# Kernel tuning notes

Measured on AMD Instinct MI355X. Metric: run time of the kernel, lower is better.

The kernel has to match this reference:

```python
import jax, jax.numpy as jnp
import numpy as np

B = 262144
N = 1_000_000
R = 64
H = 128


def setup_inputs() -> dict:
    key = jax.random.key(0)
    k1, k2, k3, k4, k5, k6 = jax.random.split(key, 6)
    return {
        "x": jax.random.randint(k1, (B,), 0, N),
        "y": jax.random.randint(k2, (B,), 0, N),
        "r": jax.random.randint(k3, (B,), 0, R),
        "l": jax.random.randint(k4, (B,), 0, 2),
        "Wx": jax.random.normal(k5, (N, H), dtype=jnp.float32),
        "Wr": jax.random.normal(k6, (R, H), dtype=jnp.float32),
    }


def reference(x, y, r, l, Wx, Wr):
    # one_hot(idx) @ W  ==  gather rows  (same math, no dense GEMM)
    embx = Wx[x]          # [B, H]
    emby = Wx[y]          # [B, H]
    embr = Wr[r]          # [B, H]

    # regulartion: sigmoid'(clamp(embr))
    s = jax.nn.sigmoid(jnp.clip(embr, -6.0, 6.0))
    re_embr = s * (1.0 - s)

    preds = jax.nn.sigmoid(jnp.sum(embx * emby * re_embr, axis=1))[:, None]  # [B,1]
    logits = jnp.concatenate([preds, 1.0 - preds], axis=1)                   # [B,2]

    # torch.nn.CrossEntropyLoss: mean(-log_softmax(logits)[i, l_i])
    log_probs = jax.nn.log_softmax(logits, axis=1)
    loss = -jnp.mean(jnp.take_along_axis(log_probs, l[:, None], axis=1))
    return logits, loss
```

## Files before the change

### kernel.cpp

```cpp
#include <hip/hip_runtime.h>
#include <math.h>


#define H_DIM 128

__global__ __launch_bounds__(256) void prep_kernel(
    const float* __restrict__ Wr, float* __restrict__ REW,
    float* __restrict__ loss_out)
{
    for (int i = threadIdx.x; i < 64 * H_DIM; i += 256) {
        const float v = fminf(6.0f, fmaxf(-6.0f, Wr[i]));
        const float s = 1.0f / (1.0f + __expf(-v));
        REW[i] = s * (1.0f - s);
    }
    if (threadIdx.x == 0) *loss_out = 0.0f;
}

#define GLOAD(it, av, bv, wv)                                          \
  {                                                                    \
    const int xi_ = __shfl(vxy, (it), 32);                             \
    const int yi_ = __shfl(vxy, 16 + (it), 32);                        \
    const int ri_ = __shfl(vr, (it), 32);                              \
    av = *(const float4*)(Wx + (size_t)xi_ * H_DIM + lane * 4);        \
    bv = *(const float4*)(Wx + (size_t)yi_ * H_DIM + lane * 4);        \
    wv = *(const float4*)(REW + (size_t)ri_ * H_DIM + lane * 4);       \
  }

#define GCOMP(it, av, bv, wv)                                          \
  {                                                                    \
    float d = (av).x * (bv).x * (wv).x + (av).y * (bv).y * (wv).y      \
            + (av).z * (bv).z * (wv).z + (av).w * (bv).w * (wv).w;     \
    d += __shfl_xor(d, 16, 64);                                        \
    d += __shfl_xor(d, 8, 64);                                         \
    d += __shfl_xor(d, 4, 64);                                         \
    d += __shfl_xor(d, 2, 64);                                         \
    d += __shfl_xor(d, 1, 64);                                         \
    if (lane == 0) dots[rbase + (it)] = d;                             \
  }

__global__ __launch_bounds__(256, 8) void gather_dot_kernel(
    const int* __restrict__ x, const int* __restrict__ y,
    const int* __restrict__ r, const float* __restrict__ Wx,
    const float* __restrict__ REW, float* __restrict__ dots, int B)
{
    const int group = threadIdx.x >> 5;
    const int lane  = threadIdx.x & 31;
    const int rbase = blockIdx.x * 128 + group * 16;

    int vxy = 0, vr = 0;
    {
        const int i = rbase + (lane & 15);
        if (i < B) {
            vxy = (lane < 16) ? x[i] : y[i];
            vr  = r[i];
        }
    }

    if (rbase + 16 <= B) {
        float4 a0, b0, w0, a1, b1, w1;
        GLOAD(0, a0, b0, w0)
        GLOAD(1, a1, b1, w1)
        #pragma unroll
        for (int it = 0; it < 14; it += 2) {
            GCOMP(it, a0, b0, w0)
            GLOAD(it + 2, a0, b0, w0)
            GCOMP(it + 1, a1, b1, w1)
            GLOAD(it + 3, a1, b1, w1)
        }
        GCOMP(14, a0, b0, w0)
        GCOMP(15, a1, b1, w1)
    } else if (rbase < B) {
        for (int it = 0; it < 16; ++it) {
            if (rbase + it >= B) break;
            float4 ta, tb, tw;
            GLOAD(it, ta, tb, tw)
            GCOMP(it, ta, tb, tw)
        }
    }
}

__global__ __launch_bounds__(256) void epilogue_kernel(
    const float* __restrict__ dots, const int* __restrict__ l,
    float* __restrict__ logits, float* __restrict__ loss_out,
    int B, float invB)
{
    float acc = 0.0f;
    for (int i = blockIdx.x * 256 + threadIdx.x; i < B;
         i += gridDim.x * 256) {
        const float d = dots[i];
        const float p = 1.0f / (1.0f + __expf(-d));
        const float q = 1.0f - p;
        *(float2*)(logits + (size_t)i * 2) = make_float2(p, q);
        const float lse = __logf(__expf(p) + __expf(q));
        acc += lse - (l[i] == 0 ? p : q);
    }
    __shared__ float sd[256];
    sd[threadIdx.x] = acc;
    __syncthreads();
    for (int s = 128; s > 0; s >>= 1) {
        if ((int)threadIdx.x < s) sd[threadIdx.x] += sd[threadIdx.x + s];
        __syncthreads();
    }
    if (threadIdx.x == 0) atomicAdd(loss_out, sd[0] * invB);
}

extern "C" void kernel_launch(void* const* d_in, const int* in_sizes, int n_in,
                              void* d_out, int out_size, void* d_ws,
                              size_t ws_size, hipStream_t stream) {
    const int*   x  = (const int*)d_in[0];
    const int*   y  = (const int*)d_in[1];
    const int*   r  = (const int*)d_in[2];
    const int*   l  = (const int*)d_in[3];
    const float* Wx = (const float*)d_in[4];
    const float* Wr = (const float*)d_in[5];

    const int B = in_sizes[0];

    float* logits   = (float*)d_out;
    float* loss_out = logits + (size_t)B * 2;

    float* REW  = (float*)d_ws;
    float* dots = REW + 64 * H_DIM;

    prep_kernel<<<1, 256, 0, stream>>>(Wr, REW, loss_out);

    const int NBLK = (B + 127) >> 7;
    gather_dot_kernel<<<NBLK, 256, 0, stream>>>(x, y, r, Wx, REW, dots, B);

    epilogue_kernel<<<512, 256, 0, stream>>>(dots, l, logits, loss_out, B,
                                             1.0f / (float)B);
}
```

Before: 631.2 us.

## Fuse prep, gather-dot and epilogue into one kernel with per-block LDS weights

Merges the relation-weight preprocessing, the gather-dot and the sigmoid/loss epilogue into a single kernel. Each block recomputes the sigmoid-derivative table into shared memory and writes per-block loss partials, and a tiny kernel then reduces them in double precision. This removes the intermediate dots buffer round trip and two launches. In exchange every block redoes the table transform, uses 32 KB of LDS, which lowers occupancy, and adds a barrier before the gathers.

```diff
diff --git a/kernel.cpp b/kernel.cpp
--- a/kernel.cpp
+++ b/kernel.cpp
@@ -3,18 +3,6 @@
 
 
 #define H_DIM 128
-
-__global__ __launch_bounds__(256) void prep_kernel(
-    const float* __restrict__ Wr, float* __restrict__ REW,
-    float* __restrict__ loss_out)
-{
-    for (int i = threadIdx.x; i < 64 * H_DIM; i += 256) {
-        const float v = fminf(6.0f, fmaxf(-6.0f, Wr[i]));
-        const float s = 1.0f / (1.0f + __expf(-v));
-        REW[i] = s * (1.0f - s);
-    }
-    if (threadIdx.x == 0) *loss_out = 0.0f;
-}
 
 #define GLOAD(it, av, bv, wv)                                          \
   {                                                                    \
@@ -23,11 +11,12 @@
     const int ri_ = __shfl(vr, (it), 32);                              \
     av = *(const float4*)(Wx + (size_t)xi_ * H_DIM + lane * 4);        \
     bv = *(const float4*)(Wx + (size_t)yi_ * H_DIM + lane * 4);        \
-    wv = *(const float4*)(REW + (size_t)ri_ * H_DIM + lane * 4);       \
+    wv = *(const float4*)(rew + ri_ * H_DIM + lane * 4);               \
   }
 
 #define GCOMP(it, av, bv, wv)                                          \
   {                                                                    \
+    const int li_ = __shfl(vl, (it), 32);                              \
     float d = (av).x * (bv).x * (wv).x + (av).y * (bv).y * (wv).y      \
             + (av).z * (bv).z * (wv).z + (av).w * (bv).w * (wv).w;     \
     d += __shfl_xor(d, 16, 64);                                        \
@@ -35,24 +24,59 @@
     d += __shfl_xor(d, 4, 64);                                         \
     d += __shfl_xor(d, 2, 64);                                         \
     d += __shfl_xor(d, 1, 64);                                         \
-    if (lane == 0) dots[rbase + (it)] = d;                             \
+    if (lane == 0) {                                                   \
+      const float p = 1.0f / (1.0f + __expf(-d));                      \
+      const float q = 1.0f - p;                                        \
+      *(float2*)(logits + (size_t)(rbase + (it)) * 2) =                \
+          make_float2(p, q);                                           \
+      const float lse = __logf(__expf(p) + __expf(q));                 \
+      lossacc += lse - (li_ == 0 ? p : q);                             \
+    }                                                                  \
   }
 
-__global__ __launch_bounds__(256, 8) void gather_dot_kernel(
+__global__ __launch_bounds__(256) void fused_kernel(
     const int* __restrict__ x, const int* __restrict__ y,
-    const int* __restrict__ r, const float* __restrict__ Wx,
-    const float* __restrict__ REW, float* __restrict__ dots, int B)
+    const int* __restrict__ r, const int* __restrict__ l,
+    const float* __restrict__ Wx, const float* __restrict__ Wr,
+    float* __restrict__ logits, float* __restrict__ partials, int B)
 {
+    __shared__ float rew[64 * H_DIM];
+    __shared__ float sloss[8];
+
+    for (int i = threadIdx.x; i < 64 * H_DIM / 4; i += 256) {
+        const float4 w4 = ((const float4*)Wr)[i];
+        float4 o;
+        {
+            const float v0 = fminf(6.0f, fmaxf(-6.0f, w4.x));
+            const float v1 = fminf(6.0f, fmaxf(-6.0f, w4.y));
+            const float v2 = fminf(6.0f, fmaxf(-6.0f, w4.z));
+            const float v3 = fminf(6.0f, fmaxf(-6.0f, w4.w));
+            const float s0 = 1.0f / (1.0f + __expf(-v0));
+            const float s1 = 1.0f / (1.0f + __expf(-v1));
+            const float s2 = 1.0f / (1.0f + __expf(-v2));
+            const float s3 = 1.0f / (1.0f + __expf(-v3));
+            o.x = s0 * (1.0f - s0);
+            o.y = s1 * (1.0f - s1);
+            o.z = s2 * (1.0f - s2);
+            o.w = s3 * (1.0f - s3);
+        }
+        ((float4*)rew)[i] = o;
+    }
+    __syncthreads();
+
     const int group = threadIdx.x >> 5;
     const int lane  = threadIdx.x & 31;
     const int rbase = blockIdx.x * 128 + group * 16;
 
-    int vxy = 0, vr = 0;
+    float lossacc = 0.0f;
+
+    int vxy = 0, vr = 0, vl = 0;
     {
         const int i = rbase + (lane & 15);
         if (i < B) {
             vxy = (lane < 16) ? x[i] : y[i];
             vr  = r[i];
+            vl  = l[i];
         }
     }
 
@@ -77,31 +101,31 @@
             GCOMP(it, ta, tb, tw)
         }
     }
+
+    if (lane == 0) sloss[group] = lossacc;
+    __syncthreads();
+    if (threadIdx.x == 0) {
+        float s = 0.0f;
+        #pragma unroll
+        for (int gi = 0; gi < 8; ++gi) s += sloss[gi];
+        partials[blockIdx.x] = s;
+    }
 }
 
-__global__ __launch_bounds__(256) void epilogue_kernel(
-    const float* __restrict__ dots, const int* __restrict__ l,
-    float* __restrict__ logits, float* __restrict__ loss_out,
-    int B, float invB)
+__global__ __launch_bounds__(256) void reduce_kernel(
+    const float* __restrict__ partials, int n, float* __restrict__ out,
+    double invB)
 {
-    float acc = 0.0f;
-    for (int i = blockIdx.x * 256 + threadIdx.x; i < B;
-         i += gridDim.x * 256) {
-        const float d = dots[i];
-        const float p = 1.0f / (1.0f + __expf(-d));
-        const float q = 1.0f - p;
-        *(float2*)(logits + (size_t)i * 2) = make_float2(p, q);
-        const float lse = __logf(__expf(p) + __expf(q));
-        acc += lse - (l[i] == 0 ? p : q);
-    }
-    __shared__ float sd[256];
+    __shared__ double sd[256];
+    double acc = 0.0;
+    for (int i = threadIdx.x; i < n; i += 256) acc += (double)partials[i];
     sd[threadIdx.x] = acc;
     __syncthreads();
     for (int s = 128; s > 0; s >>= 1) {
         if ((int)threadIdx.x < s) sd[threadIdx.x] += sd[threadIdx.x + s];
         __syncthreads();
     }
-    if (threadIdx.x == 0) atomicAdd(loss_out, sd[0] * invB);
+    if (threadIdx.x == 0) *out = (float)(sd[0] * invB);
 }
 
 extern "C" void kernel_launch(void* const* d_in, const int* in_sizes, int n_in,
@@ -119,14 +143,11 @@
     float* logits   = (float*)d_out;
     float* loss_out = logits + (size_t)B * 2;
 
-    float* REW  = (float*)d_ws;
-    float* dots = REW + 64 * H_DIM;
+    float* partials = (float*)d_ws;
+    const int NBLK = (B + 127) >> 7;
 
-    prep_kernel<<<1, 256, 0, stream>>>(Wr, REW, loss_out);
-
-    const int NBLK = (B + 127) >> 7;
-    gather_dot_kernel<<<NBLK, 256, 0, stream>>>(x, y, r, Wx, REW, dots, B);
-
-    epilogue_kernel<<<512, 256, 0, stream>>>(dots, l, logits, loss_out, B,
-                                             1.0f / (float)B);
+    fused_kernel<<<NBLK, 256, 0, stream>>>(x, y, r, l, Wx, Wr, logits,
+                                           partials, B);
+    reduce_kernel<<<1, 256, 0, stream>>>(partials, NBLK, loss_out,
+                                         1.0 / (double)B);
 }
```

Result: faster. 618.6 us (-2.0%).
